# Kernel tuning notes

Hardware: AMD Instinct MI355X
Metric: run time of the kernel (lower is better)

## Reference

```python
import jax, jax.numpy as jnp
import numpy as np

N_NODES = 50000
N_GRAPHS = 32
NODE_F = 16
GLOBAL_F = 2
HID = 300
LAT = 100
N_EDGES = 800000


def _glorot(key, shape):
    fan_in, fan_out = shape[0], shape[1]
    s = jnp.sqrt(2.0 / (fan_in + fan_out))
    return jax.random.normal(key, shape, dtype=jnp.float32) * s


def setup_inputs() -> dict:
    key = jax.random.key(0)
    ks = jax.random.split(key, 24)
    x = jax.random.normal(ks[0], (N_NODES, NODE_F), dtype=jnp.float32)
    edge_index = jax.random.randint(ks[1], (2, N_EDGES), 0, N_NODES, dtype=jnp.int64)
    batch = jnp.sort(jax.random.randint(ks[2], (N_NODES,), 0, N_GRAPHS, dtype=jnp.int64))
    u = jax.random.normal(ks[3], (N_GRAPHS, GLOBAL_F), dtype=jnp.float32)
    # layer 0: in=NODE_F, layer 1: in=LAT
    p = {}
    p['l0_w1'] = _glorot(ks[4], (2 * NODE_F, HID)); p['l0_b1'] = jnp.zeros((HID,), jnp.float32)
    p['l0_w2'] = _glorot(ks[5], (HID, HID));        p['l0_b2'] = jnp.zeros((HID,), jnp.float32)
    p['l0_w3'] = _glorot(ks[6], (HID, LAT));        p['l0_b3'] = jnp.zeros((LAT,), jnp.float32)
    p['l1_w1'] = _glorot(ks[7], (2 * LAT, HID));    p['l1_b1'] = jnp.zeros((HID,), jnp.float32)
    p['l1_w2'] = _glorot(ks[8], (HID, HID));        p['l1_b2'] = jnp.zeros((HID,), jnp.float32)
    p['l1_w3'] = _glorot(ks[9], (HID, LAT));        p['l1_b3'] = jnp.zeros((LAT,), jnp.float32)
    p['lin_w1'] = _glorot(ks[10], (LAT + GLOBAL_F, LAT)); p['lin_b1'] = jnp.zeros((LAT,), jnp.float32)
    p['lin_w2'] = _glorot(ks[11], (LAT, LAT));            p['lin_b2'] = jnp.zeros((LAT,), jnp.float32)
    p['lin_w3'] = _glorot(ks[12], (LAT, 1));              p['lin_b3'] = jnp.zeros((1,), jnp.float32)
    return dict(x=x, edge_index=edge_index, batch=batch, u=u, **p)


def _edge_layer(x, src, dst, w1, b1, w2, b2, w3, b3):
    # gather endpoints; torch_geometric default flow: x_j = x[src], x_i = x[dst]
    xi = x[dst]
    xj = x[src]
    inp = jnp.concatenate([xi, xj - xi], axis=-1)          # [E, 2*in]
    h = jax.nn.relu(inp @ w1 + b1)
    h = jax.nn.relu(h @ w2 + b2)
    m = h @ w3 + b3                                         # [E, out]
    s = jax.ops.segment_sum(m, dst, num_segments=N_NODES)  # scatter-sum to target nodes
    cnt = jax.ops.segment_sum(jnp.ones((m.shape[0],), m.dtype), dst, num_segments=N_NODES)
    return s / jnp.maximum(cnt, 1.0)[:, None]               # scatter-mean


def _mean_pool(x, batch):
    s = jax.ops.segment_sum(x, batch, num_segments=N_GRAPHS)
    cnt = jax.ops.segment_sum(jnp.ones((x.shape[0],), x.dtype), batch, num_segments=N_GRAPHS)
    return s / jnp.maximum(cnt, 1.0)[:, None]


def reference(x, edge_index, batch, u,
              l0_w1, l0_b1, l0_w2, l0_b2, l0_w3, l0_b3,
              l1_w1, l1_b1, l1_w2, l1_b2, l1_w3, l1_b3,
              lin_w1, lin_b1, lin_w2, lin_b2, lin_w3, lin_b3):
    src, dst = edge_index[0], edge_index[1]
    x = _edge_layer(x, src, dst, l0_w1, l0_b1, l0_w2, l0_b2, l0_w3, l0_b3)
    x = jax.nn.relu(x)
    x = _edge_layer(x, src, dst, l1_w1, l1_b1, l1_w2, l1_b2, l1_w3, l1_b3)
    x = jax.nn.relu(x)
    pooled = jnp.concatenate([_mean_pool(x, batch), u], axis=1)  # [G, LAT+GLOBAL_F]
    h = jax.nn.relu(pooled @ lin_w1 + lin_b1)
    h = jax.nn.relu(h @ lin_w2 + lin_b2)
    return h @ lin_w3 + lin_b3  # [G, 1]
```

## Files before the change

### kernel.cpp

```cpp
#include <hip/hip_runtime.h>
#include <cstdint>
#include <cstddef>

#define N_NODES  50000
#define N_GRAPHS 32
#define NODE_F   16
#define GLOBAL_F 2
#define HID      300
#define LAT      100
#define N_EDGES  800000

#define HIDP 320
#define LATP 128
#define NCT1 (HIDP/16)
#define NCT2 (LATP/16)
#define NKS  (HIDP/32)
#define EPB  64
#define ROWP 66
#define HSFS 132

#define W2F_ELEMS 102400
#define W3F_ELEMS 40960
#define W1F0_ELEMS 20480
#define W1F1_ELEMS 81920

typedef __bf16 bf16x8 __attribute__((ext_vector_type(8)));
typedef float  f32x4  __attribute__((ext_vector_type(4)));

__device__ __forceinline__ float relu_f(float x){ return fmaxf(x, 0.f); }

__device__ __forceinline__ unsigned short f2bf(float x){
  unsigned int u = __float_as_uint(x);
  u = (u + 0x7FFFu + ((u >> 16) & 1u)) >> 16;
  return (unsigned short)u;
}
__device__ __forceinline__ unsigned short f2bf_hw(float x){
  __bf16 h = (__bf16)x;
  return __builtin_bit_cast(unsigned short, h);
}
__device__ __forceinline__ float bf2f(unsigned int h){
  return __uint_as_float(h << 16);
}

__device__ __forceinline__ void pack_one(const float* __restrict__ w, int K, int N,
                                         int nct, unsigned short* __restrict__ out, int i){
  int j  = i & 7;
  int l  = (i >> 3) & 63;
  int t  = i >> 9;
  int ct = t % nct, ks = t / nct;
  int n = ct*16 + (l & 15);
  int k = ks*32 + ((l >> 4) << 3) + j;
  float v = (k < K && n < N) ? w[(size_t)k*N + n] : 0.f;
  out[i] = f2bf(v);
}

__device__ __forceinline__ void pack_w1_one(const float* __restrict__ w1, int F,
                                            unsigned short* __restrict__ out, int i){
  int j  = i & 7;
  int l  = (i >> 3) & 63;
  int t  = i >> 9;
  int ct = t % 40, ks = t / 40;
  int n = ct*16 + (l & 15);
  int k = ks*32 + ((l >> 4) << 3) + j;
  float v = 0.f;
  if (k < F){
    if (n < HIDP){ if (n < HID) v = w1[(size_t)k*HID + n] - w1[(size_t)(F+k)*HID + n]; }
    else { int nn = n - HIDP; if (nn < HID) v = w1[(size_t)(F+k)*HID + nn]; }
  }
  out[i] = f2bf(v);
}

#define PR_B0 (N_NODES*LAT + N_NODES)
#define PR_B1 (PR_B0 + 2*W2F_ELEMS + 2*W3F_ELEMS)
#define PR_B2 (PR_B1 + W1F0_ELEMS)
#define PR_B3 (PR_B2 + W1F1_ELEMS)
#define PR_B4 (PR_B3 + HIDP)
#define PR_B5 (PR_B4 + N_NODES*32)

__global__ void prep_kernel(
    int* __restrict__ zero_region,
    const float* __restrict__ w2a, const float* __restrict__ w3a,
    const float* __restrict__ w2b, const float* __restrict__ w3b,
    unsigned short* __restrict__ o2a, unsigned short* __restrict__ o3a,
    unsigned short* __restrict__ o2b, unsigned short* __restrict__ o3b,
    const float* __restrict__ w1a, unsigned short* __restrict__ o1a,
    const float* __restrict__ w1b, unsigned short* __restrict__ o1b,
    const float* __restrict__ ba0, const float* __restrict__ ba1,
    const float* __restrict__ ba2, const float* __restrict__ ba3,
    float* __restrict__ bo0, float* __restrict__ bo1,
    float* __restrict__ bo2, float* __restrict__ bo3,
    const float* __restrict__ x, unsigned short* __restrict__ xb){
  int i = blockIdx.x*blockDim.x + threadIdx.x;
  if (i < PR_B0){ zero_region[i] = 0; return; }
  if (i < PR_B1){
    int t = i - PR_B0;
    if (t < W2F_ELEMS) pack_one(w2a, HID, HID, NCT1, o2a, t);
    else if (t < W2F_ELEMS + W3F_ELEMS) pack_one(w3a, HID, LAT, NCT2, o3a, t - W2F_ELEMS);
    else if (t < 2*W2F_ELEMS + W3F_ELEMS) pack_one(w2b, HID, HID, NCT1, o2b, t - W2F_ELEMS - W3F_ELEMS);
    else pack_one(w3b, HID, LAT, NCT2, o3b, t - 2*W2F_ELEMS - W3F_ELEMS);
    return;
  }
  if (i < PR_B2){ pack_w1_one(w1a, NODE_F, o1a, i - PR_B1); return; }
  if (i < PR_B3){ pack_w1_one(w1b, LAT,    o1b, i - PR_B2); return; }
  if (i < PR_B4){
    int t = i - PR_B3;
    bo0[t] = (t < HID) ? ba0[t] : 0.f;
    bo1[t] = (t < HID) ? ba1[t] : 0.f;
    bo2[t] = (t < HID) ? ba2[t] : 0.f;
    bo3[t] = (t < HID) ? ba3[t] : 0.f;
    return;
  }
  if (i < PR_B5){
    int t = i - PR_B4;
    int n = t >> 5, c = t & 31;
    xb[t] = (c < NODE_F) ? f2bf(x[(size_t)n*NODE_F + c]) : 0;
    return;
  }
}

__global__ void hist_kernel(const int* __restrict__ ei, int* __restrict__ hist){
  int e = blockIdx.x*blockDim.x + threadIdx.x;
  if (e < N_EDGES) atomicAdd(&hist[ei[N_EDGES + e]], 1);
}

__global__ __launch_bounds__(256) void scan_kernel(const int* __restrict__ hist,
                                                   int* __restrict__ woff){
  __shared__ int part[256];
  const int t = threadIdx.x;
  const int CH = (N_NODES + 255) / 256;
  const int lo = t*CH, hi = (lo + CH < N_NODES) ? lo + CH : N_NODES;
  int s = 0;
  for (int i = lo; i < hi; ++i) s += hist[i];
  part[t] = s;
  __syncthreads();
  for (int d = 1; d < 256; d <<= 1){
    int v = (t >= d) ? part[t-d] : 0;
    __syncthreads();
    part[t] += v;
    __syncthreads();
  }
  int run = (t == 0) ? 0 : part[t-1];
  for (int i = lo; i < hi; ++i){ woff[i] = run; run += hist[i]; }
}

__global__ void sort_gstart(const int* __restrict__ ei, int* __restrict__ woff,
                            int* __restrict__ es, int* __restrict__ ed,
                            const int* __restrict__ batch, int* __restrict__ gstart){
  int e = blockIdx.x*blockDim.x + threadIdx.x;
  if (e < N_EDGES){
    int s = ei[e], d = ei[N_EDGES + e];
    int pos = atomicAdd(&woff[d], 1);
    es[pos] = s; ed[pos] = d;
  }
  if (e < N_NODES){
    int n = e;
    int b = batch[n];
    if (n == 0){ for (int g = 0; g <= b; ++g) gstart[g] = 0; }
    else {
      int bp = batch[n-1];
      for (int g = bp+1; g <= b; ++g) gstart[g] = n;
    }
    if (n == N_NODES-1){ for (int g = b+1; g <= N_GRAPHS; ++g) gstart[g] = N_NODES; }
  }
}

template<int KPAD>
__global__ __launch_bounds__(256) void node_gemm(
    const unsigned short* __restrict__ xb, const unsigned short* __restrict__ wf,
    unsigned short* __restrict__ Ub, unsigned short* __restrict__ Vb){
  constexpr int NCH = KPAD/8;
  __shared__ __align__(16) unsigned short at[NCH][66][8];
  const int tid = threadIdx.x;
  const int n0 = blockIdx.x*64;
  for (int i = tid; i < 64*NCH; i += 256){
    int row = i / NCH, c = i % NCH;
    int n = n0 + row; if (n >= N_NODES) n = N_NODES-1;
    *(uint4*)&at[c][row][0] = *(const uint4*)&xb[(size_t)n*KPAD + c*8];
  }
  __syncthreads();
  const int wave = tid >> 6, l = tid & 63;
  const int lrow = l & 15, lq = l >> 4;
  f32x4 acc[4][10];
  #pragma unroll
  for (int rt = 0; rt < 4; ++rt)
    #pragma unroll
    for (int c = 0; c < 10; ++c)
      acc[rt][c] = (f32x4){0.f,0.f,0.f,0.f};
  for (int ks = 0; ks < KPAD/32; ++ks){
    bf16x8 a[4];
    #pragma unroll
    for (int rt = 0; rt < 4; ++rt)
      a[rt] = __builtin_bit_cast(bf16x8, *(const uint4*)&at[4*ks + lq][16*rt + lrow][0]);
    #pragma unroll
    for (int c = 0; c < 10; ++c){
      int ct = wave*10 + c;
      bf16x8 b = __builtin_bit_cast(bf16x8,
                   *(const uint4*)&wf[(((size_t)(ks*40 + ct)) << 9) + l*8]);
      #pragma unroll
      for (int rt = 0; rt < 4; ++rt)
        acc[rt][c] = __builtin_amdgcn_mfma_f32_16x16x32_bf16(a[rt], b, acc[rt][c], 0, 0, 0);
    }
  }
  #pragma unroll
  for (int c = 0; c < 10; ++c){
    int col = (wave*10 + c)*16 + lrow;
    #pragma unroll
    for (int rt = 0; rt < 4; ++rt){
      #pragma unroll
      for (int r = 0; r < 4; ++r){
        int n = n0 + rt*16 + lq*4 + r;
        if (n < N_NODES){
          unsigned short hv = f2bf_hw(acc[rt][c][r]);
          if (col < HIDP) Ub[(size_t)n*HIDP + col] = hv;
          else            Vb[(size_t)n*HIDP + col - HIDP] = hv;
        }
      }
    }
  }
}

__global__ __launch_bounds__(256, 3) void edge_mfma(
    const int* __restrict__ es, const int* __restrict__ ed,
    const unsigned short* __restrict__ U, const unsigned short* __restrict__ V,
    const float* __restrict__ b1p, const unsigned short* __restrict__ w2f,
    const float* __restrict__ b2p, const unsigned short* __restrict__ w3f,
    float* __restrict__ nodeacc){
  __shared__ __align__(16) unsigned char smem[(HIDP/8)*ROWP*8*2];
  __shared__ int sdst[EPB];
  __shared__ int sflag[EPB];
  unsigned short* hsb = (unsigned short*)smem;
  float*          hsf = (float*)smem;
  #define HS(c,row) (hsb + (((c)*ROWP + (row)) << 3))

  const int tid = threadIdx.x;
  const int e0 = blockIdx.x * EPB;
  const int eL = tid & 63;
  const int mysrc = es[e0 + eL];
  const int mydst = ed[e0 + eL];
  if (tid < EPB) sdst[tid] = mydst;

  const size_t ubase = (size_t)mydst*HIDP;
  const size_t vbase = (size_t)mysrc*HIDP;
  #pragma unroll
  for (int it = 0; it < 10; ++it){
    int c = (tid + it*256) >> 6;
    const uint4 uu = *(const uint4*)&U[ubase + c*8];
    const uint4 vv = *(const uint4*)&V[vbase + c*8];
    const float4 bl = *(const float4*)&b1p[c*8];
    const float4 bh = *(const float4*)&b1p[c*8 + 4];
    const unsigned int uarr[4] = {uu.x, uu.y, uu.z, uu.w};
    const unsigned int varr[4] = {vv.x, vv.y, vv.z, vv.w};
    const float barr[8] = {bl.x, bl.y, bl.z, bl.w, bh.x, bh.y, bh.z, bh.w};
    unsigned int ou[4];
    #pragma unroll
    for (int q = 0; q < 4; ++q){
      float f0 = relu_f(bf2f(uarr[q] & 0xFFFFu) + bf2f(varr[q] & 0xFFFFu) + barr[2*q]);
      float f1 = relu_f(bf2f(uarr[q] >> 16)     + bf2f(varr[q] >> 16)     + barr[2*q+1]);
      ou[q] = (unsigned int)f2bf_hw(f0) | ((unsigned int)f2bf_hw(f1) << 16);
    }
    *(uint4*)HS(c, eL) = make_uint4(ou[0], ou[1], ou[2], ou[3]);
  }
  __syncthreads();

  const int wave = tid >> 6, l = tid & 63;
  const int lrow = l & 15, lq = l >> 4;

  f32x4 acc1[4][5];
  #pragma unroll
  for (int rt = 0; rt < 4; ++rt)
    #pragma unroll
    for (int c = 0; c < 5; ++c)
      acc1[rt][c] = (f32x4){0.f,0.f,0.f,0.f};
  for (int ks = 0; ks < NKS; ++ks){
    bf16x8 a[4];
    #pragma unroll
    for (int rt = 0; rt < 4; ++rt)
      a[rt] = __builtin_bit_cast(bf16x8, *(const uint4*)HS(4*ks + lq, 16*rt + lrow));
    #pragma unroll
    for (int c = 0; c < 5; ++c){
      int ct = wave*5 + c;
      bf16x8 b = __builtin_bit_cast(bf16x8,
                   *(const uint4*)&w2f[(((size_t)(ks*NCT1 + ct)) << 9) + l*8]);
      #pragma unroll
      for (int rt = 0; rt < 4; ++rt)
        acc1[rt][c] = __builtin_amdgcn_mfma_f32_16x16x32_bf16(a[rt], b, acc1[rt][c], 0, 0, 0);
    }
  }
  __syncthreads();

  #pragma unroll
  for (int c = 0; c < 5; ++c){
    int col = (wave*5 + c)*16 + lrow;
    float b2v = b2p[col];
    #pragma unroll
    for (int rt = 0; rt < 4; ++rt){
      #pragma unroll
      for (int r = 0; r < 4; ++r){
        int row = rt*16 + lq*4 + r;
        HS(col >> 3, row)[col & 7] = f2bf_hw(relu_f(acc1[rt][c][r] + b2v));
      }
    }
  }
  __syncthreads();

  f32x4 acc2[4][2];
  #pragma unroll
  for (int rt = 0; rt < 4; ++rt)
    #pragma unroll
    for (int c = 0; c < 2; ++c)
      acc2[rt][c] = (f32x4){0.f,0.f,0.f,0.f};
  for (int ks = 0; ks < NKS; ++ks){
    bf16x8 a[4];
    #pragma unroll
    for (int rt = 0; rt < 4; ++rt)
      a[rt] = __builtin_bit_cast(bf16x8, *(const uint4*)HS(4*ks + lq, 16*rt + lrow));
    #pragma unroll
    for (int c = 0; c < 2; ++c){
      int ct = wave*2 + c;
      bf16x8 b = __builtin_bit_cast(bf16x8,
                   *(const uint4*)&w3f[(((size_t)(ks*NCT2 + ct)) << 9) + l*8]);
      #pragma unroll
      for (int rt = 0; rt < 4; ++rt)
        acc2[rt][c] = __builtin_amdgcn_mfma_f32_16x16x32_bf16(a[rt], b, acc2[rt][c], 0, 0, 0);
    }
  }
  __syncthreads();

  #pragma unroll
  for (int c = 0; c < 2; ++c){
    int col = (wave*2 + c)*16 + lrow;
    #pragma unroll
    for (int rt = 0; rt < 4; ++rt){
      #pragma unroll
      for (int r = 0; r < 4; ++r){
        int row = rt*16 + lq*4 + r;
        hsf[row*HSFS + col] = acc2[rt][c][r];
      }
    }
  }
  if (tid < EPB) sflag[tid] = (tid == 0) || (sdst[tid] != sdst[tid-1]);
  __syncthreads();

  {
    const int col = tid & 127;
    if (col < LAT){
      for (int s = tid >> 7; s < EPB; s += 2){
        if (!sflag[s]) continue;
        int d = sdst[s];
        float sum = hsf[s*HSFS + col];
        int r = s + 1;
        while (r < EPB && !sflag[r]){ sum += hsf[r*HSFS + col]; ++r; }
        atomicAdd(&nodeacc[(size_t)d*LAT + col], sum);
      }
    }
  }
  #undef HS
}

__global__ void finalize_kernel(float* __restrict__ nodeacc, const int* __restrict__ hist,
                                const float* __restrict__ b3,
                                unsigned short* __restrict__ x1b){
  int idx = blockIdx.x*blockDim.x + threadIdx.x;
  if (idx < N_NODES*128){
    int n = idx >> 7, j = idx & 127;
    unsigned short o = 0;
    if (j < LAT){
      int c = hist[n];
      float v = nodeacc[(size_t)n*LAT + j] / fmaxf((float)c, 1.f);
      v += (c > 0) ? b3[j] : 0.f;
      o = f2bf_hw(relu_f(v));
      nodeacc[(size_t)n*LAT + j] = 0.f;
    }
    x1b[idx] = o;
  }
}

__global__ __launch_bounds__(512) void pool_seg(const unsigned short* __restrict__ x1b,
                                                const int* __restrict__ gstart,
                                                float* __restrict__ pooled){
  __shared__ float buf[3][128];
  const int g = blockIdx.x;
  const int lo = gstart[g], hi = gstart[g+1];
  const int col = threadIdx.x & 127, q = threadIdx.x >> 7;
  float s = 0.f;
  for (int n = lo + q; n < hi; n += 4) s += bf2f(x1b[(size_t)n*128 + col]);
  if (q) buf[q-1][col] = s;
  __syncthreads();
  if (q == 0 && col < LAT){
    float tot = s + buf[0][col] + buf[1][col] + buf[2][col];
    pooled[g*LAT + col] = tot / fmaxf((float)(hi - lo), 1.f);
  }
}

__global__ __launch_bounds__(128) void head_kernel(
    const float* __restrict__ pooled,
    const float* __restrict__ u,
    const float* __restrict__ w1, const float* __restrict__ bb1,
    const float* __restrict__ w2, const float* __restrict__ bb2,
    const float* __restrict__ w3, const float* __restrict__ bb3,
    float* __restrict__ out){
  __shared__ float p[N_GRAPHS][LAT+GLOBAL_F];
  __shared__ float h1[N_GRAPHS][LAT];
  __shared__ float h2[N_GRAPHS][LAT];
  const int tid = threadIdx.x;
  for (int t = tid; t < N_GRAPHS*LAT; t += 128){
    int g = t / LAT, k = t - g*LAT;
    p[g][k] = pooled[t];
  }
  for (int t = tid; t < N_GRAPHS*GLOBAL_F; t += 128){
    int g = t / GLOBAL_F, c = t - g*GLOBAL_F;
    p[g][LAT + c] = u[t];
  }
  __syncthreads();
  for (int t = tid; t < N_GRAPHS*LAT; t += 128){
    int g = t / LAT, j = t - g*LAT;
    float s = bb1[j];
    for (int k = 0; k < LAT+GLOBAL_F; k++) s += p[g][k]*w1[(size_t)k*LAT + j];
    h1[g][j] = relu_f(s);
  }
  __syncthreads();
  for (int t = tid; t < N_GRAPHS*LAT; t += 128){
    int g = t / LAT, j = t - g*LAT;
    float s = bb2[j];
    for (int k = 0; k < LAT; k++) s += h1[g][k]*w2[(size_t)k*LAT + j];
    h2[g][j] = relu_f(s);
  }
  __syncthreads();
  for (int t = tid; t < N_GRAPHS; t += 128){
    float s = bb3[0];
    for (int k = 0; k < LAT; k++) s += h2[t][k]*w3[k];
    out[t] = s;
  }
}

extern "C" void kernel_launch(void* const* d_in, const int* in_sizes, int n_in,
                              void* d_out, int out_size, void* d_ws, size_t ws_size,
                              hipStream_t stream){
  (void)in_sizes; (void)n_in; (void)out_size; (void)ws_size;
  const float* x     = (const float*)d_in[0];
  const int*   ei    = (const int*)d_in[1];
  const int*   batch = (const int*)d_in[2];
  const float* u     = (const float*)d_in[3];
  const float* l0_w1 = (const float*)d_in[4];  const float* l0_b1 = (const float*)d_in[5];
  const float* l0_w2 = (const float*)d_in[6];  const float* l0_b2 = (const float*)d_in[7];
  const float* l0_w3 = (const float*)d_in[8];  const float* l0_b3 = (const float*)d_in[9];
  const float* l1_w1 = (const float*)d_in[10]; const float* l1_b1 = (const float*)d_in[11];
  const float* l1_w2 = (const float*)d_in[12]; const float* l1_b2 = (const float*)d_in[13];
  const float* l1_w3 = (const float*)d_in[14]; const float* l1_b3 = (const float*)d_in[15];
  const float* lin_w1= (const float*)d_in[16]; const float* lin_b1= (const float*)d_in[17];
  const float* lin_w2= (const float*)d_in[18]; const float* lin_b2= (const float*)d_in[19];
  const float* lin_w3= (const float*)d_in[20]; const float* lin_b3= (const float*)d_in[21];

  char* wsb = (char*)d_ws;
  const size_t UV_BYTES = (size_t)N_NODES*HIDP*sizeof(unsigned short);

  unsigned short* Ub   = (unsigned short*)wsb;  wsb += UV_BYTES;
  unsigned short* Vb   = (unsigned short*)wsb;  wsb += UV_BYTES;
  unsigned short* w2f0 = (unsigned short*)wsb;  wsb += (size_t)W2F_ELEMS*2;
  unsigned short* w3f0 = (unsigned short*)wsb;  wsb += (size_t)W3F_ELEMS*2;
  unsigned short* w2f1 = (unsigned short*)wsb;  wsb += (size_t)W2F_ELEMS*2;
  unsigned short* w3f1 = (unsigned short*)wsb;  wsb += (size_t)W3F_ELEMS*2;
  unsigned short* w1f0 = (unsigned short*)wsb;  wsb += (size_t)W1F0_ELEMS*2;
  unsigned short* w1f1 = (unsigned short*)wsb;  wsb += (size_t)W1F1_ELEMS*2;
  float* b1p0 = (float*)wsb;                    wsb += HIDP*4;
  float* b2p0 = (float*)wsb;                    wsb += HIDP*4;
  float* b1p1 = (float*)wsb;                    wsb += HIDP*4;
  float* b2p1 = (float*)wsb;                    wsb += HIDP*4;
  unsigned short* xb0 = (unsigned short*)wsb;   wsb += (size_t)N_NODES*32*2;
  unsigned short* x1b = (unsigned short*)wsb;   wsb += (size_t)N_NODES*128*2;
  float* nodeacc = (float*)wsb;                 wsb += (size_t)N_NODES*LAT*4;
  int*   hist    = (int*)wsb;                   wsb += (size_t)N_NODES*4;
  int*   woff    = (int*)wsb;                   wsb += (size_t)N_NODES*4;
  int*   es      = (int*)wsb;                   wsb += (size_t)N_EDGES*4;
  int*   ed      = (int*)wsb;                   wsb += (size_t)N_EDGES*4;
  int*   gstart  = (int*)wsb;                   wsb += 64*4;
  float* pooled  = (float*)wsb;                 wsb += (size_t)N_GRAPHS*LAT*4;

  hipLaunchKernelGGL(prep_kernel, dim3((PR_B5+255)/256), dim3(256), 0, stream,
                     (int*)nodeacc,
                     l0_w2, l0_w3, l1_w2, l1_w3, w2f0, w3f0, w2f1, w3f1,
                     l0_w1, w1f0, l1_w1, w1f1,
                     l0_b1, l0_b2, l1_b1, l1_b2, b1p0, b2p0, b1p1, b2p1,
                     x, xb0);
  hipLaunchKernelGGL(hist_kernel, dim3((N_EDGES+255)/256), dim3(256), 0, stream, ei, hist);
  hipLaunchKernelGGL(scan_kernel, dim3(1), dim3(256), 0, stream, hist, woff);
  hipLaunchKernelGGL(sort_gstart, dim3((N_EDGES+255)/256), dim3(256), 0, stream,
                     ei, woff, es, ed, batch, gstart);

  const int NGB = (N_NODES + 63)/64;
  const int NEB = N_EDGES/EPB;

  hipLaunchKernelGGL(node_gemm<32>, dim3(NGB), dim3(256), 0, stream, xb0, w1f0, Ub, Vb);
  hipLaunchKernelGGL(edge_mfma, dim3(NEB), dim3(256), 0, stream,
                     es, ed, Ub, Vb, b1p0, w2f0, b2p0, w3f0, nodeacc);
  hipLaunchKernelGGL(finalize_kernel, dim3((N_NODES*128+255)/256), dim3(256), 0, stream,
                     nodeacc, hist, l0_b3, x1b);

  hipLaunchKernelGGL(node_gemm<128>, dim3(NGB), dim3(256), 0, stream, x1b, w1f1, Ub, Vb);
  hipLaunchKernelGGL(edge_mfma, dim3(NEB), dim3(256), 0, stream,
                     es, ed, Ub, Vb, b1p1, w2f1, b2p1, w3f1, nodeacc);
  hipLaunchKernelGGL(finalize_kernel, dim3((N_NODES*128+255)/256), dim3(256), 0, stream,
                     nodeacc, hist, l1_b3, x1b);

  hipLaunchKernelGGL(pool_seg, dim3(N_GRAPHS), dim3(512), 0, stream, x1b, gstart, pooled);
  hipLaunchKernelGGL(head_kernel, dim3(1), dim3(128), 0, stream,
                     pooled, u, lin_w1, lin_b1, lin_w2, lin_b2, lin_w3, lin_b3,
                     (float*)d_out);
}
```

Baseline: 1.495 ms.

## Pack edge indices, fold bias into node GEMM, swizzle edge LDS tiles

Packs the sorted src/dst edge indices into one int2 array. The first-layer bias moves into the node GEMM epilogue, so the edge kernel no longer loads b1 per chunk. The edge kernel's LDS tile switches from row padding to an XOR swizzle, gathers are software-prefetched one chunk ahead, shared sdst/sflag arrays are replaced by wavefront shuffles, and the occupancy hint rises from 3 to 4 blocks. The final finalize pass also skips re-zeroing the accumulator. These aim to cut gather and LDS overhead and raise occupancy, at the risk of register spills under the tighter launch bound.

```diff
diff --git a/kernel.cpp b/kernel.cpp
--- a/kernel.cpp
+++ b/kernel.cpp
@@ -16,7 +16,6 @@
 #define NCT2 (LATP/16)
 #define NKS  (HIDP/32)
 #define EPB  64
-#define ROWP 66
 #define HSFS 132
 
 #define W2F_ELEMS 102400
@@ -144,13 +143,13 @@
 }
 
 __global__ void sort_gstart(const int* __restrict__ ei, int* __restrict__ woff,
-                            int* __restrict__ es, int* __restrict__ ed,
+                            int2* __restrict__ esd,
                             const int* __restrict__ batch, int* __restrict__ gstart){
   int e = blockIdx.x*blockDim.x + threadIdx.x;
   if (e < N_EDGES){
     int s = ei[e], d = ei[N_EDGES + e];
     int pos = atomicAdd(&woff[d], 1);
-    es[pos] = s; ed[pos] = d;
+    esd[pos] = make_int2(s, d);
   }
   if (e < N_NODES){
     int n = e;
@@ -167,6 +166,7 @@
 template<int KPAD>
 __global__ __launch_bounds__(256) void node_gemm(
     const unsigned short* __restrict__ xb, const unsigned short* __restrict__ wf,
+    const float* __restrict__ b1p,
     unsigned short* __restrict__ Ub, unsigned short* __restrict__ Vb){
   constexpr int NCH = KPAD/8;
   __shared__ __align__(16) unsigned short at[NCH][66][8];
@@ -204,61 +204,62 @@
   #pragma unroll
   for (int c = 0; c < 10; ++c){
     int col = (wave*10 + c)*16 + lrow;
+    const bool isU = (col < HIDP);
+    const float bv = isU ? b1p[col] : 0.f;
     #pragma unroll
     for (int rt = 0; rt < 4; ++rt){
       #pragma unroll
       for (int r = 0; r < 4; ++r){
         int n = n0 + rt*16 + lq*4 + r;
         if (n < N_NODES){
-          unsigned short hv = f2bf_hw(acc[rt][c][r]);
-          if (col < HIDP) Ub[(size_t)n*HIDP + col] = hv;
-          else            Vb[(size_t)n*HIDP + col - HIDP] = hv;
+          if (isU) Ub[(size_t)n*HIDP + col] = f2bf_hw(acc[rt][c][r] + bv);
+          else     Vb[(size_t)n*HIDP + col - HIDP] = f2bf_hw(acc[rt][c][r]);
         }
       }
     }
   }
 }
 
-__global__ __launch_bounds__(256, 3) void edge_mfma(
-    const int* __restrict__ es, const int* __restrict__ ed,
+__global__ __launch_bounds__(256, 4) void edge_mfma(
+    const int2* __restrict__ esd,
     const unsigned short* __restrict__ U, const unsigned short* __restrict__ V,
-    const float* __restrict__ b1p, const unsigned short* __restrict__ w2f,
+    const unsigned short* __restrict__ w2f,
     const float* __restrict__ b2p, const unsigned short* __restrict__ w3f,
     float* __restrict__ nodeacc){
-  __shared__ __align__(16) unsigned char smem[(HIDP/8)*ROWP*8*2];
-  __shared__ int sdst[EPB];
-  __shared__ int sflag[EPB];
-  unsigned short* hsb = (unsigned short*)smem;
-  float*          hsf = (float*)smem;
-  #define HS(c,row) (hsb + (((c)*ROWP + (row)) << 3))
+  __shared__ __align__(16) unsigned short hsb[40*64*8];
+  float* hsf = (float*)hsb;
+  #define HS(c,row) (hsb + (((((c)<<6)) + (((row) ^ (((c)&3)<<2)))) << 3))
 
   const int tid = threadIdx.x;
   const int e0 = blockIdx.x * EPB;
   const int eL = tid & 63;
-  const int mysrc = es[e0 + eL];
-  const int mydst = ed[e0 + eL];
-  if (tid < EPB) sdst[tid] = mydst;
-
-  const size_t ubase = (size_t)mydst*HIDP;
-  const size_t vbase = (size_t)mysrc*HIDP;
+  const int2 se = esd[e0 + eL];
+  const int mysrc = se.x, mydst = se.y;
+
+  const size_t ub = (size_t)mydst*HIDP;
+  const size_t vb = (size_t)mysrc*HIDP;
+  const int c0 = tid >> 6;
+  uint4 uu = *(const uint4*)&U[ub + c0*8];
+  uint4 vv = *(const uint4*)&V[vb + c0*8];
   #pragma unroll
   for (int it = 0; it < 10; ++it){
-    int c = (tid + it*256) >> 6;
-    const uint4 uu = *(const uint4*)&U[ubase + c*8];
-    const uint4 vv = *(const uint4*)&V[vbase + c*8];
-    const float4 bl = *(const float4*)&b1p[c*8];
-    const float4 bh = *(const float4*)&b1p[c*8 + 4];
-    const unsigned int uarr[4] = {uu.x, uu.y, uu.z, uu.w};
-    const unsigned int varr[4] = {vv.x, vv.y, vv.z, vv.w};
-    const float barr[8] = {bl.x, bl.y, bl.z, bl.w, bh.x, bh.y, bh.z, bh.w};
+    const int c = c0 + it*4;
+    uint4 uun, vvn;
+    if (it < 9){
+      uun = *(const uint4*)&U[ub + (size_t)(c+4)*8];
+      vvn = *(const uint4*)&V[vb + (size_t)(c+4)*8];
+    }
+    const unsigned int ua[4] = {uu.x,uu.y,uu.z,uu.w};
+    const unsigned int va[4] = {vv.x,vv.y,vv.z,vv.w};
     unsigned int ou[4];
     #pragma unroll
     for (int q = 0; q < 4; ++q){
-      float f0 = relu_f(bf2f(uarr[q] & 0xFFFFu) + bf2f(varr[q] & 0xFFFFu) + barr[2*q]);
-      float f1 = relu_f(bf2f(uarr[q] >> 16)     + bf2f(varr[q] >> 16)     + barr[2*q+1]);
+      float f0 = relu_f(bf2f(ua[q] & 0xFFFFu) + bf2f(va[q] & 0xFFFFu));
+      float f1 = relu_f(bf2f(ua[q] >> 16)     + bf2f(va[q] >> 16));
       ou[q] = (unsigned int)f2bf_hw(f0) | ((unsigned int)f2bf_hw(f1) << 16);
     }
     *(uint4*)HS(c, eL) = make_uint4(ou[0], ou[1], ou[2], ou[3]);
+    if (it < 9){ uu = uun; vv = vvn; }
   }
   __syncthreads();
 
@@ -338,20 +339,20 @@
       }
     }
   }
-  if (tid < EPB) sflag[tid] = (tid == 0) || (sdst[tid] != sdst[tid-1]);
   __syncthreads();
 
   {
     const int col = tid & 127;
-    if (col < LAT){
-      for (int s = tid >> 7; s < EPB; s += 2){
-        if (!sflag[s]) continue;
-        int d = sdst[s];
-        float sum = hsf[s*HSFS + col];
-        int r = s + 1;
-        while (r < EPB && !sflag[r]){ sum += hsf[r*HSFS + col]; ++r; }
-        atomicAdd(&nodeacc[(size_t)d*LAT + col], sum);
+    for (int s = tid >> 7; s < EPB; s += 2){
+      int d  = __shfl(mydst, s, 64);
+      int dp = __shfl(mydst, (s > 0) ? (s - 1) : 0, 64);
+      if (s > 0 && d == dp) continue;
+      float sum = hsf[s*HSFS + col];
+      int r = s + 1;
+      while (r < EPB && __shfl(mydst, r, 64) == d){
+        sum += hsf[r*HSFS + col]; ++r;
       }
+      if (col < LAT) atomicAdd(&nodeacc[(size_t)d*LAT + col], sum);
     }
   }
   #undef HS
@@ -359,7 +360,7 @@
 
 __global__ void finalize_kernel(float* __restrict__ nodeacc, const int* __restrict__ hist,
                                 const float* __restrict__ b3,
-                                unsigned short* __restrict__ x1b){
+                                unsigned short* __restrict__ x1b, int rezero){
   int idx = blockIdx.x*blockDim.x + threadIdx.x;
   if (idx < N_NODES*128){
     int n = idx >> 7, j = idx & 127;
@@ -369,7 +370,7 @@
       float v = nodeacc[(size_t)n*LAT + j] / fmaxf((float)c, 1.f);
       v += (c > 0) ? b3[j] : 0.f;
       o = f2bf_hw(relu_f(v));
-      nodeacc[(size_t)n*LAT + j] = 0.f;
+      if (rezero) nodeacc[(size_t)n*LAT + j] = 0.f;
     }
     x1b[idx] = o;
   }
@@ -471,8 +472,7 @@
   float* nodeacc = (float*)wsb;                 wsb += (size_t)N_NODES*LAT*4;
   int*   hist    = (int*)wsb;                   wsb += (size_t)N_NODES*4;
   int*   woff    = (int*)wsb;                   wsb += (size_t)N_NODES*4;
-  int*   es      = (int*)wsb;                   wsb += (size_t)N_EDGES*4;
-  int*   ed      = (int*)wsb;                   wsb += (size_t)N_EDGES*4;
+  int2*  esd     = (int2*)wsb;                  wsb += (size_t)N_EDGES*8;
   int*   gstart  = (int*)wsb;                   wsb += 64*4;
   float* pooled  = (float*)wsb;                 wsb += (size_t)N_GRAPHS*LAT*4;
 
@@ -485,22 +485,24 @@
   hipLaunchKernelGGL(hist_kernel, dim3((N_EDGES+255)/256), dim3(256), 0, stream, ei, hist);
   hipLaunchKernelGGL(scan_kernel, dim3(1), dim3(256), 0, stream, hist, woff);
   hipLaunchKernelGGL(sort_gstart, dim3((N_EDGES+255)/256), dim3(256), 0, stream,
-                     ei, woff, es, ed, batch, gstart);
+                     ei, woff, esd, batch, gstart);
 
   const int NGB = (N_NODES + 63)/64;
   const int NEB = N_EDGES/EPB;
 
-  hipLaunchKernelGGL(node_gemm<32>, dim3(NGB), dim3(256), 0, stream, xb0, w1f0, Ub, Vb);
+  hipLaunchKernelGGL(node_gemm<32>, dim3(NGB), dim3(256), 0, stream,
+                     xb0, w1f0, b1p0, Ub, Vb);
   hipLaunchKernelGGL(edge_mfma, dim3(NEB), dim3(256), 0, stream,
-                     es, ed, Ub, Vb, b1p0, w2f0, b2p0, w3f0, nodeacc);
+                     esd, Ub, Vb, w2f0, b2p0, w3f0, nodeacc);
   hipLaunchKernelGGL(finalize_kernel, dim3((N_NODES*128+255)/256), dim3(256), 0, stream,
-                     nodeacc, hist, l0_b3, x1b);
-
-  hipLaunchKernelGGL(node_gemm<128>, dim3(NGB), dim3(256), 0, stream, x1b, w1f1, Ub, Vb);
+                     nodeacc, hist, l0_b3, x1b, 1);
+
+  hipLaunchKernelGGL(node_gemm<128>, dim3(NGB), dim3(256), 0, stream,
+                     x1b, w1f1, b1p1, Ub, Vb);
   hipLaunchKernelGGL(edge_mfma, dim3(NEB), dim3(256), 0, stream,
-                     es, ed, Ub, Vb, b1p1, w2f1, b2p1, w3f1, nodeacc);
+                     esd, Ub, Vb, w2f1, b2p1, w3f1, nodeacc);
   hipLaunchKernelGGL(finalize_kernel, dim3((N_NODES*128+255)/256), dim3(256), 0, stream,
-                     nodeacc, hist, l1_b3, x1b);
+                     nodeacc, hist, l1_b3, x1b, 0);
 
   hipLaunchKernelGGL(pool_seg, dim3(N_GRAPHS), dim3(512), 0, stream, x1b, gstart, pooled);
   hipLaunchKernelGGL(head_kernel, dim3(1), dim3(128), 0, stream,
```

Measured after the change: 1.734 ms. 16.0% more time.
